# Kernel tuning notes

Hardware: AMD Instinct MI355X
Metric: run time of the kernel (lower is better)

The kernel has to match this reference:

```python
import jax, jax.numpy as jnp
import numpy as np

EPS = 1e-5  # BatchNorm eps (eval mode with running stats)

def conv1x1(x, w, b):
    # 1x1x1 Conv3d == channel matmul. x: (b,c,t,h,w), w: (o,c), b: (o,)
    return jnp.einsum('bcthw,oc->bothw', x, w) + b[None, :, None, None, None]

def pool122(x):
    # MaxPool3d kernel (1,2,2): max over non-overlapping 2x2 spatial windows
    b, c, t, h, w = x.shape
    return x.reshape(b, c, t, h // 2, 2, w // 2, 2).max(axis=(4, 6))

def setup_inputs() -> dict:
    key = jax.random.key(0)
    ks = jax.random.split(key, 13)
    C, Ci = 256, 128
    f32 = jnp.float32
    rn = lambda k, s, sc=1.0: jax.random.normal(k, s, dtype=f32) * sc
    return {
        'x': rn(ks[0], (4, C, 8, 32, 32)),
        'g_w': rn(ks[1], (Ci, C), 0.05), 'g_b': rn(ks[2], (Ci,), 0.05),
        'theta_w': rn(ks[3], (Ci, C), 0.05), 'theta_b': rn(ks[4], (Ci,), 0.05),
        'phi_w': rn(ks[5], (Ci, C), 0.05), 'phi_b': rn(ks[6], (Ci,), 0.05),
        'w_w': rn(ks[7], (C, Ci), 0.05), 'w_b': rn(ks[8], (C,), 0.05),
        'bn_gamma': rn(ks[9], (C,), 0.1) + 1.0,
        'bn_beta': rn(ks[10], (C,), 0.1),
        'bn_mean': rn(ks[11], (C,), 0.1),
        'bn_var': jax.random.uniform(ks[12], (C,), dtype=f32, minval=0.5, maxval=1.5),
    }

def reference(x, g_w, g_b, theta_w, theta_b, phi_w, phi_b, w_w, w_b,
              bn_gamma, bn_beta, bn_mean, bn_var):
    b = x.shape[0]
    ci = g_w.shape[0]
    # g, phi: conv then (1,2,2) maxpool (sub_sample=True)
    g_x = pool122(conv1x1(x, g_w, g_b)).reshape(b, ci, -1).transpose(0, 2, 1)      # (b, Nkv, ci)
    theta_x = conv1x1(x, theta_w, theta_b).reshape(b, ci, -1).transpose(0, 2, 1)   # (b, Nq, ci)
    phi_x = pool122(conv1x1(x, phi_w, phi_b)).reshape(b, ci, -1)                    # (b, ci, Nkv)
    f = jnp.einsum('bnc,bcm->bnm', theta_x, phi_x)                                  # (b, Nq, Nkv)
    attn = jax.nn.softmax(f, axis=-1)
    yy = jnp.einsum('bnm,bmc->bnc', attn, g_x)                                      # (b, Nq, ci)
    yy = yy.transpose(0, 2, 1).reshape(b, ci, *x.shape[2:])                         # (b, ci, t, h, w)
    wy = conv1x1(yy, w_w, w_b)
    # BatchNorm3d in eval mode with running stats
    scale = bn_gamma * jax.lax.rsqrt(bn_var + EPS)
    wy = wy * scale[None, :, None, None, None] + (bn_beta - bn_mean * scale)[None, :, None, None, None]
    return wy + x
```

## Files before the change

kernel.cpp:

```cpp
#include <hip/hip_runtime.h>
#include <hip/hip_bf16.h>

typedef __bf16 bf16x8 __attribute__((ext_vector_type(8)));
typedef __bf16 bf16x4 __attribute__((ext_vector_type(4)));
typedef __bf16 bf16x2 __attribute__((ext_vector_type(2)));
typedef float  f32x4  __attribute__((ext_vector_type(4)));

#define NB   4
#define C_   256
#define CI_  128
#define NSP  8192
#define NKV  2048
#define KVT  32
#define NT   (NKV/KVT)

__device__ __forceinline__ void gload_lds16(const void* g, void* l) {
    __builtin_amdgcn_global_load_lds(
        (const __attribute__((address_space(1))) void*)(unsigned long long)(uintptr_t)g,
        (__attribute__((address_space(3))) void*)(unsigned)(uintptr_t)l,
        16, 0, 0);
}

__global__ __launch_bounds__(256) void prep_kernel(
    const float* __restrict__ g_w,  const float* __restrict__ g_b,
    const float* __restrict__ th_w, const float* __restrict__ th_b,
    const float* __restrict__ ph_w, const float* __restrict__ ph_b,
    const float* __restrict__ w_w,  const float* __restrict__ w_b,
    const float* __restrict__ bn_g, const float* __restrict__ bn_be,
    const float* __restrict__ bn_m, const float* __restrict__ bn_v,
    __bf16* __restrict__ w_all, __bf16* __restrict__ w2,
    float* __restrict__ b_all, float* __restrict__ bnA, float* __restrict__ bnB)
{
    int idx = blockIdx.x * 256 + threadIdx.x;
    if (idx < 98304) {
        int o = idx >> 8, c = idx & 255;
        float v;
        if (o < 128)      v = th_w[o*256 + c];
        else if (o < 256) v = ph_w[(o-128)*256 + c];
        else              v = g_w[(o-256)*256 + c];
        w_all[idx] = (__bf16)v;
    } else if (idx < 131072) {
        int j = idx - 98304;
        w2[j] = (__bf16)w_w[j];
    } else if (idx < 131456) {
        int k = idx - 131072;
        float v;
        if (k < 128) v = th_b[k]; else if (k < 256) v = ph_b[k-128]; else v = g_b[k-256];
        b_all[k] = v;
    } else if (idx < 131712) {
        int m = idx - 131456;
        float sc = bn_g[m] * rsqrtf(bn_v[m] + 1e-5f);
        bnA[m] = sc;
        bnB[m] = w_b[m]*sc + bn_be[m] - bn_m[m]*sc;
    }
}

__global__ __launch_bounds__(256, 2) void proj_kernel(
    const float* __restrict__ x, const __bf16* __restrict__ w_all,
    const float* __restrict__ b_all,
    __bf16* __restrict__ Q, __bf16* __restrict__ K, __bf16* __restrict__ VT)
{
    const int b    = blockIdx.x >> 7;
    const int tile = blockIdx.x & 127;
    const int n0   = tile * 64;
    const int w    = threadIdx.x >> 6;
    const int lane = threadIdx.x & 63;
    const int lq   = lane & 15;
    const int g    = lane >> 4;

    const float* xb = x + b * (C_ * NSP);

    f32x4 acc[4][6];
    #pragma unroll
    for (int a = 0; a < 4; ++a)
        #pragma unroll
        for (int o = 0; o < 6; ++o) acc[a][o] = (f32x4){0.f,0.f,0.f,0.f};

    #pragma unroll 1
    for (int ck = 0; ck < 8; ++ck) {
        const int cbase = ck*32 + g*8;
        bf16x8 afr[4];
        #pragma unroll
        for (int nf = 0; nf < 4; ++nf) {
            const int n = n0 + nf*16 + lq;
            const float* xp = xb + cbase*NSP + n;
            bf16x8 v;
            #pragma unroll
            for (int e = 0; e < 8; ++e) v[e] = (__bf16)xp[e*NSP];
            afr[nf] = v;
        }
        #pragma unroll
        for (int oi = 0; oi < 6; ++oi) {
            const int orow = (w*6 + oi)*16 + lq;
            bf16x8 bfr = *(const bf16x8*)(w_all + orow*256 + cbase);
            #pragma unroll
            for (int nf = 0; nf < 4; ++nf)
                acc[nf][oi] = __builtin_amdgcn_mfma_f32_16x16x32_bf16(afr[nf], bfr, acc[nf][oi], 0,0,0);
        }
    }

    const int t  = n0 >> 10;
    const int h0 = (n0 & 1023) >> 5;
    const int kvrow0 = t*256 + (h0 >> 1)*16;

    #pragma unroll
    for (int oi = 0; oi < 6; ++oi) {
        const int ocol = (w*6 + oi)*16 + lq;
        const float bias = b_all[ocol];
        float v[4][4];
        #pragma unroll
        for (int nf = 0; nf < 4; ++nf)
            #pragma unroll
            for (int i = 0; i < 4; ++i) v[nf][i] = acc[nf][oi][i] + bias;

        const int seg = ocol >> 7;
        const int ol  = ocol & 127;
        if (seg == 0) {
            #pragma unroll
            for (int nf = 0; nf < 4; ++nf)
                #pragma unroll
                for (int i = 0; i < 4; ++i) {
                    int n = n0 + nf*16 + g*4 + i;
                    Q[(b*NSP + n)*CI_ + ol] = (__bf16)v[nf][i];
                }
        } else if (seg == 1) {
            #pragma unroll
            for (int nfp = 0; nfp < 2; ++nfp)
                #pragma unroll
                for (int j = 0; j < 2; ++j) {
                    float pv = fmaxf(fmaxf(v[nfp][2*j], v[nfp][2*j+1]),
                                     fmaxf(v[nfp+2][2*j], v[nfp+2][2*j+1]));
                    int wp = nfp*8 + g*2 + j;
                    K[(b*NKV + kvrow0 + wp)*CI_ + ol] = (__bf16)pv;
                }
        } else {
            #pragma unroll
            for (int nfp = 0; nfp < 2; ++nfp) {
                bf16x2 pk;
                #pragma unroll
                for (int j = 0; j < 2; ++j) {
                    float pv = fmaxf(fmaxf(v[nfp][2*j], v[nfp][2*j+1]),
                                     fmaxf(v[nfp+2][2*j], v[nfp+2][2*j+1]));
                    pk[j] = (__bf16)pv;
                }
                int wp = nfp*8 + g*2;
                *(bf16x2*)(VT + (b*CI_ + ol)*NKV + kvrow0 + wp) = pk;
            }
        }
    }
}

__global__ __launch_bounds__(256, 2) void attn_kernel(
    const __bf16* __restrict__ Q, const __bf16* __restrict__ K,
    const __bf16* __restrict__ VT, __bf16* __restrict__ yy)
{
    __shared__ __bf16 kbuf[3][32*128];
    __shared__ __bf16 vbuf[3][128*32];
    __shared__ __bf16 plds[4][16][40];

    const int b    = blockIdx.x >> 7;
    const int qt   = blockIdx.x & 127;
    const int w    = threadIdx.x >> 6;
    const int lane = threadIdx.x & 63;
    const int lq   = lane & 15;
    const int g    = lane >> 4;
    const int q0   = qt*64 + w*16;
    const float LOG2E = 1.4426950408889634f;

    bf16x8 qf[4];
    const __bf16* qrow = Q + (size_t)(b*NSP + q0 + lq)*CI_;
    #pragma unroll
    for (int kk = 0; kk < 4; ++kk) qf[kk] = *(const bf16x8*)(qrow + kk*32 + g*8);

    float m_run = -1e30f, l_run = 0.f;
    f32x4 oacc[8];
    #pragma unroll
    for (int d = 0; d < 8; ++d) oacc[d] = (f32x4){0.f,0.f,0.f,0.f};

    const __bf16* Kb0 = K  + (size_t)b*NKV*CI_;
    const __bf16* Vb0 = VT + (size_t)b*CI_*NKV;
    __bf16* pw = &plds[w][0][0];

    auto stage = [&](int bi, int kv0) {
        #pragma unroll
        for (int j = 0; j < 2; ++j) {
            int o   = w*2048 + j*1024 + lane*16;
            int row = o >> 8;
            int c   = (o & 255) ^ ((row & 7) << 4);
            const __bf16* src = Kb0 + (size_t)(kv0 + row)*CI_ + (c >> 1);
            gload_lds16(src, (char*)&kbuf[bi][0] + w*2048 + j*1024);
        }
        #pragma unroll
        for (int j = 0; j < 2; ++j) {
            int o    = w*2048 + j*1024 + lane*16;
            int row  = o >> 6;
            int slot = (o >> 4) & 3;
            int kc   = slot ^ ((row >> 1) & 3);
            const __bf16* src = Vb0 + (size_t)row*NKV + kv0 + kc*8;
            gload_lds16(src, (char*)&vbuf[bi][0] + w*2048 + j*1024);
        }
    };

    stage(0, 0);
    stage(1, KVT);

    for (int t = 0; t < NT; ++t) {
        asm volatile("s_waitcnt vmcnt(4)" ::: "memory");
        __builtin_amdgcn_s_barrier();
        __builtin_amdgcn_sched_barrier(0);

        {
            int tn = t + 2;
            int kvn = (tn < NT ? tn : NT-1) * KVT;
            stage(tn % 3, kvn);
        }

        const int bi = t % 3;
        const char* kb = (const char*)&kbuf[bi][0];
        const char* vb = (const char*)&vbuf[bi][0];

        f32x4 facc[2] = {(f32x4){0.f,0.f,0.f,0.f}, (f32x4){0.f,0.f,0.f,0.f}};
        __builtin_amdgcn_s_setprio(1);
        #pragma unroll
        for (int kk = 0; kk < 4; ++kk) {
            #pragma unroll
            for (int nf = 0; nf < 2; ++nf) {
                int row = nf*16 + lq;
                int c   = (kk*64 + g*16) ^ ((row & 7) << 4);
                bf16x8 kf = *(const bf16x8*)(kb + row*256 + c);
                facc[nf] = __builtin_amdgcn_mfma_f32_16x16x32_bf16(kf, qf[kk], facc[nf], 0,0,0);
            }
        }
        __builtin_amdgcn_s_setprio(0);

        float m0 = fmaxf(fmaxf(facc[0][0], facc[0][1]), fmaxf(facc[0][2], facc[0][3]));
        float m1 = fmaxf(fmaxf(facc[1][0], facc[1][1]), fmaxf(facc[1][2], facc[1][3]));
        float pmax = fmaxf(m0, m1);
        pmax = fmaxf(pmax, __shfl_xor(pmax, 16, 64));
        pmax = fmaxf(pmax, __shfl_xor(pmax, 32, 64));
        if (!__all(pmax - m_run <= 8.f)) {
            float mnew = fmaxf(m_run, pmax);
            float corr = __builtin_amdgcn_exp2f((m_run - mnew) * LOG2E);
            l_run *= corr;
            #pragma unroll
            for (int d = 0; d < 8; ++d) {
                oacc[d][0] *= corr; oacc[d][1] *= corr;
                oacc[d][2] *= corr; oacc[d][3] *= corr;
            }
            m_run = mnew;
        }
        float p[8];
        #pragma unroll
        for (int nf = 0; nf < 2; ++nf)
            #pragma unroll
            for (int i = 0; i < 4; ++i)
                p[nf*4+i] = __builtin_amdgcn_exp2f((facc[nf][i] - m_run) * LOG2E);
        float ps = ((p[0]+p[1]) + (p[2]+p[3])) + ((p[4]+p[5]) + (p[6]+p[7]));
        ps += __shfl_xor(ps, 16, 64);
        ps += __shfl_xor(ps, 32, 64);
        l_run += ps;

        #pragma unroll
        for (int nf = 0; nf < 2; ++nf) {
            bf16x4 pk;
            #pragma unroll
            for (int i = 0; i < 4; ++i) pk[i] = (__bf16)p[nf*4+i];
            *(bf16x4*)(pw + lq*40 + nf*16 + g*4) = pk;
        }
        bf16x8 pb = *(const bf16x8*)(pw + lq*40 + g*8);

        __builtin_amdgcn_s_setprio(1);
        #pragma unroll
        for (int df = 0; df < 8; ++df) {
            int row = df*16 + lq;
            int cb  = (g*16) ^ (((row >> 1) & 3) << 4);
            bf16x8 vf = *(const bf16x8*)(vb + row*64 + cb);
            oacc[df] = __builtin_amdgcn_mfma_f32_16x16x32_bf16(vf, pb, oacc[df], 0,0,0);
        }
        __builtin_amdgcn_s_setprio(0);
    }

    float inv = 1.f / l_run;
    __bf16* yrow = yy + (size_t)(b*NSP + q0 + lq)*CI_;
    #pragma unroll
    for (int df = 0; df < 8; ++df) {
        bf16x4 ov;
        #pragma unroll
        for (int i = 0; i < 4; ++i) ov[i] = (__bf16)(oacc[df][i] * inv);
        *(bf16x4*)(yrow + df*16 + g*4) = ov;
    }
}

__global__ __launch_bounds__(256, 2) void out_kernel(
    const __bf16* __restrict__ yy, const __bf16* __restrict__ w2,
    const float* __restrict__ bnA, const float* __restrict__ bnB,
    const float* __restrict__ x, float* __restrict__ out)
{
    const int b    = blockIdx.x >> 7;
    const int tile = blockIdx.x & 127;
    const int n0   = tile * 64;
    const int w    = threadIdx.x >> 6;
    const int lane = threadIdx.x & 63;
    const int lq   = lane & 15;
    const int g    = lane >> 4;

    f32x4 acc[4][4];
    #pragma unroll
    for (int a = 0; a < 4; ++a)
        #pragma unroll
        for (int o = 0; o < 4; ++o) acc[a][o] = (f32x4){0.f,0.f,0.f,0.f};

    #pragma unroll
    for (int kk = 0; kk < 4; ++kk) {
        bf16x8 bfr[4];
        #pragma unroll
        for (int nf = 0; nf < 4; ++nf)
            bfr[nf] = *(const bf16x8*)(yy + (size_t)(b*NSP + n0 + nf*16 + lq)*CI_ + kk*32 + g*8);
        #pragma unroll
        for (int cf = 0; cf < 4; ++cf) {
            const int corow = (w*4 + cf)*16 + lq;
            bf16x8 afr = *(const bf16x8*)(w2 + corow*CI_ + kk*32 + g*8);
            #pragma unroll
            for (int nf = 0; nf < 4; ++nf)
                acc[cf][nf] = __builtin_amdgcn_mfma_f32_16x16x32_bf16(afr, bfr[nf], acc[cf][nf], 0,0,0);
        }
    }

    #pragma unroll
    for (int cf = 0; cf < 4; ++cf) {
        #pragma unroll
        for (int i = 0; i < 4; ++i) {
            int co = (w*4 + cf)*16 + g*4 + i;
            float A = bnA[co], Bv = bnB[co];
            #pragma unroll
            for (int nf = 0; nf < 4; ++nf) {
                int n = n0 + nf*16 + lq;
                size_t idx = (size_t)(b*C_ + co)*NSP + n;
                out[idx] = acc[cf][nf][i]*A + Bv + x[idx];
            }
        }
    }
}

extern "C" void kernel_launch(void* const* d_in, const int* in_sizes, int n_in,
                              void* d_out, int out_size, void* d_ws, size_t ws_size,
                              hipStream_t stream)
{
    const float* x    = (const float*)d_in[0];
    const float* g_w  = (const float*)d_in[1];
    const float* g_b  = (const float*)d_in[2];
    const float* th_w = (const float*)d_in[3];
    const float* th_b = (const float*)d_in[4];
    const float* ph_w = (const float*)d_in[5];
    const float* ph_b = (const float*)d_in[6];
    const float* w_w  = (const float*)d_in[7];
    const float* w_b  = (const float*)d_in[8];
    const float* bn_g = (const float*)d_in[9];
    const float* bn_be= (const float*)d_in[10];
    const float* bn_m = (const float*)d_in[11];
    const float* bn_v = (const float*)d_in[12];

    char* ws = (char*)d_ws;
    size_t off = 0;
    auto alloc = [&](size_t bytes) -> void* {
        void* p = ws + off;
        off += (bytes + 255) & ~(size_t)255;
        return p;
    };
    __bf16* w_all = (__bf16*)alloc(384*256*2);
    __bf16* w2    = (__bf16*)alloc(256*128*2);
    float*  b_all = (float*) alloc(384*4);
    float*  bnA   = (float*) alloc(256*4);
    float*  bnB   = (float*) alloc(256*4);
    __bf16* Qb    = (__bf16*)alloc((size_t)NB*NSP*CI_*2);
    __bf16* Kb    = (__bf16*)alloc((size_t)NB*NKV*CI_*2);
    __bf16* Vt    = (__bf16*)alloc((size_t)NB*CI_*NKV*2);
    __bf16* yyb   = (__bf16*)alloc((size_t)NB*NSP*CI_*2);

    prep_kernel<<<515, 256, 0, stream>>>(g_w, g_b, th_w, th_b, ph_w, ph_b, w_w, w_b,
                                         bn_g, bn_be, bn_m, bn_v,
                                         w_all, w2, b_all, bnA, bnB);
    proj_kernel<<<512, 256, 0, stream>>>(x, w_all, b_all, Qb, Kb, Vt);
    attn_kernel<<<512, 256, 0, stream>>>(Qb, Kb, Vt, yyb);
    out_kernel <<<512, 256, 0, stream>>>(yyb, w2, bnA, bnB, x, (float*)d_out);
}
```

Before: 198.6 us.

## Double query rows per wave in attention and vectorize output epilogue

Each attention wave now handles 32 query rows in two 16-row sub-tiles, so every K and V fragment read from LDS feeds two MFMAs. This halves the grid to 256 blocks and drops to one block per CU, doubling K/V reuse per LDS stage. In the output kernel the MFMA operands are swapped so each lane holds four consecutive spatial positions, which allows 16-byte vectorized loads of x and stores of out. The cost is higher register pressure and fewer blocks than CUs on MI355X, which reduces occupancy and latency hiding.

```diff
diff --git a/kernel.cpp b/kernel.cpp
--- a/kernel.cpp
+++ b/kernel.cpp
@@ -150,32 +150,37 @@
     }
 }
 
-__global__ __launch_bounds__(256, 2) void attn_kernel(
+__global__ __launch_bounds__(256, 1) void attn_kernel(
     const __bf16* __restrict__ Q, const __bf16* __restrict__ K,
     const __bf16* __restrict__ VT, __bf16* __restrict__ yy)
 {
     __shared__ __bf16 kbuf[3][32*128];
     __shared__ __bf16 vbuf[3][128*32];
-    __shared__ __bf16 plds[4][16][40];
-
-    const int b    = blockIdx.x >> 7;
-    const int qt   = blockIdx.x & 127;
+    __shared__ __bf16 plds[4][32][40];
+
+    const int b    = blockIdx.x >> 6;
+    const int qt   = blockIdx.x & 63;
     const int w    = threadIdx.x >> 6;
     const int lane = threadIdx.x & 63;
     const int lq   = lane & 15;
     const int g    = lane >> 4;
-    const int q0   = qt*64 + w*16;
+    const int q0   = qt*128 + w*32;
     const float LOG2E = 1.4426950408889634f;
 
-    bf16x8 qf[4];
-    const __bf16* qrow = Q + (size_t)(b*NSP + q0 + lq)*CI_;
-    #pragma unroll
-    for (int kk = 0; kk < 4; ++kk) qf[kk] = *(const bf16x8*)(qrow + kk*32 + g*8);
-
-    float m_run = -1e30f, l_run = 0.f;
-    f32x4 oacc[8];
-    #pragma unroll
-    for (int d = 0; d < 8; ++d) oacc[d] = (f32x4){0.f,0.f,0.f,0.f};
+    bf16x8 qf[2][4];
+    #pragma unroll
+    for (int s = 0; s < 2; ++s) {
+        const __bf16* qrow = Q + (size_t)(b*NSP + q0 + s*16 + lq)*CI_;
+        #pragma unroll
+        for (int kk = 0; kk < 4; ++kk) qf[s][kk] = *(const bf16x8*)(qrow + kk*32 + g*8);
+    }
+
+    float m_run[2] = {-1e30f, -1e30f}, l_run[2] = {0.f, 0.f};
+    f32x4 oacc[2][8];
+    #pragma unroll
+    for (int s = 0; s < 2; ++s)
+        #pragma unroll
+        for (int d = 0; d < 8; ++d) oacc[s][d] = (f32x4){0.f,0.f,0.f,0.f};
 
     const __bf16* Kb0 = K  + (size_t)b*NKV*CI_;
     const __bf16* Vb0 = VT + (size_t)b*CI_*NKV;
@@ -219,7 +224,11 @@
         const char* kb = (const char*)&kbuf[bi][0];
         const char* vb = (const char*)&vbuf[bi][0];
 
-        f32x4 facc[2] = {(f32x4){0.f,0.f,0.f,0.f}, (f32x4){0.f,0.f,0.f,0.f}};
+        f32x4 facc[2][2];
+        #pragma unroll
+        for (int s = 0; s < 2; ++s)
+            #pragma unroll
+            for (int nf = 0; nf < 2; ++nf) facc[s][nf] = (f32x4){0.f,0.f,0.f,0.f};
         __builtin_amdgcn_s_setprio(1);
         #pragma unroll
         for (int kk = 0; kk < 4; ++kk) {
@@ -228,46 +237,52 @@
                 int row = nf*16 + lq;
                 int c   = (kk*64 + g*16) ^ ((row & 7) << 4);
                 bf16x8 kf = *(const bf16x8*)(kb + row*256 + c);
-                facc[nf] = __builtin_amdgcn_mfma_f32_16x16x32_bf16(kf, qf[kk], facc[nf], 0,0,0);
+                facc[0][nf] = __builtin_amdgcn_mfma_f32_16x16x32_bf16(kf, qf[0][kk], facc[0][nf], 0,0,0);
+                facc[1][nf] = __builtin_amdgcn_mfma_f32_16x16x32_bf16(kf, qf[1][kk], facc[1][nf], 0,0,0);
             }
         }
         __builtin_amdgcn_s_setprio(0);
 
-        float m0 = fmaxf(fmaxf(facc[0][0], facc[0][1]), fmaxf(facc[0][2], facc[0][3]));
-        float m1 = fmaxf(fmaxf(facc[1][0], facc[1][1]), fmaxf(facc[1][2], facc[1][3]));
-        float pmax = fmaxf(m0, m1);
-        pmax = fmaxf(pmax, __shfl_xor(pmax, 16, 64));
-        pmax = fmaxf(pmax, __shfl_xor(pmax, 32, 64));
-        if (!__all(pmax - m_run <= 8.f)) {
-            float mnew = fmaxf(m_run, pmax);
-            float corr = __builtin_amdgcn_exp2f((m_run - mnew) * LOG2E);
-            l_run *= corr;
-            #pragma unroll
-            for (int d = 0; d < 8; ++d) {
-                oacc[d][0] *= corr; oacc[d][1] *= corr;
-                oacc[d][2] *= corr; oacc[d][3] *= corr;
+        #pragma unroll
+        for (int s = 0; s < 2; ++s) {
+            float m0 = fmaxf(fmaxf(facc[s][0][0], facc[s][0][1]), fmaxf(facc[s][0][2], facc[s][0][3]));
+            float m1 = fmaxf(fmaxf(facc[s][1][0], facc[s][1][1]), fmaxf(facc[s][1][2], facc[s][1][3]));
+            float pmax = fmaxf(m0, m1);
+            pmax = fmaxf(pmax, __shfl_xor(pmax, 16, 64));
+            pmax = fmaxf(pmax, __shfl_xor(pmax, 32, 64));
+            if (!__all(pmax - m_run[s] <= 8.f)) {
+                float mnew = fmaxf(m_run[s], pmax);
+                float corr = __builtin_amdgcn_exp2f((m_run[s] - mnew) * LOG2E);
+                l_run[s] *= corr;
+                #pragma unroll
+                for (int d = 0; d < 8; ++d) {
+                    oacc[s][d][0] *= corr; oacc[s][d][1] *= corr;
+                    oacc[s][d][2] *= corr; oacc[s][d][3] *= corr;
+                }
+                m_run[s] = mnew;
             }
-            m_run = mnew;
-        }
-        float p[8];
-        #pragma unroll
-        for (int nf = 0; nf < 2; ++nf)
-            #pragma unroll
-            for (int i = 0; i < 4; ++i)
-                p[nf*4+i] = __builtin_amdgcn_exp2f((facc[nf][i] - m_run) * LOG2E);
-        float ps = ((p[0]+p[1]) + (p[2]+p[3])) + ((p[4]+p[5]) + (p[6]+p[7]));
-        ps += __shfl_xor(ps, 16, 64);
-        ps += __shfl_xor(ps, 32, 64);
-        l_run += ps;
-
-        #pragma unroll
-        for (int nf = 0; nf < 2; ++nf) {
-            bf16x4 pk;
-            #pragma unroll
-            for (int i = 0; i < 4; ++i) pk[i] = (__bf16)p[nf*4+i];
-            *(bf16x4*)(pw + lq*40 + nf*16 + g*4) = pk;
-        }
-        bf16x8 pb = *(const bf16x8*)(pw + lq*40 + g*8);
+            float p[8];
+            #pragma unroll
+            for (int nf = 0; nf < 2; ++nf)
+                #pragma unroll
+                for (int i = 0; i < 4; ++i)
+                    p[nf*4+i] = __builtin_amdgcn_exp2f((facc[s][nf][i] - m_run[s]) * LOG2E);
+            float ps = ((p[0]+p[1]) + (p[2]+p[3])) + ((p[4]+p[5]) + (p[6]+p[7]));
+            ps += __shfl_xor(ps, 16, 64);
+            ps += __shfl_xor(ps, 32, 64);
+            l_run[s] += ps;
+            #pragma unroll
+            for (int nf = 0; nf < 2; ++nf) {
+                bf16x4 pk;
+                #pragma unroll
+                for (int i = 0; i < 4; ++i) pk[i] = (__bf16)p[nf*4+i];
+                *(bf16x4*)(pw + (s*16 + lq)*40 + nf*16 + g*4) = pk;
+            }
+        }
+        bf16x8 pb[2];
+        #pragma unroll
+        for (int s = 0; s < 2; ++s)
+            pb[s] = *(const bf16x8*)(pw + (s*16 + lq)*40 + g*8);
 
         __builtin_amdgcn_s_setprio(1);
         #pragma unroll
@@ -275,19 +290,23 @@
             int row = df*16 + lq;
             int cb  = (g*16) ^ (((row >> 1) & 3) << 4);
             bf16x8 vf = *(const bf16x8*)(vb + row*64 + cb);
-            oacc[df] = __builtin_amdgcn_mfma_f32_16x16x32_bf16(vf, pb, oacc[df], 0,0,0);
+            oacc[0][df] = __builtin_amdgcn_mfma_f32_16x16x32_bf16(vf, pb[0], oacc[0][df], 0,0,0);
+            oacc[1][df] = __builtin_amdgcn_mfma_f32_16x16x32_bf16(vf, pb[1], oacc[1][df], 0,0,0);
         }
         __builtin_amdgcn_s_setprio(0);
     }
 
-    float inv = 1.f / l_run;
-    __bf16* yrow = yy + (size_t)(b*NSP + q0 + lq)*CI_;
-    #pragma unroll
-    for (int df = 0; df < 8; ++df) {
-        bf16x4 ov;
-        #pragma unroll
-        for (int i = 0; i < 4; ++i) ov[i] = (__bf16)(oacc[df][i] * inv);
-        *(bf16x4*)(yrow + df*16 + g*4) = ov;
+    #pragma unroll
+    for (int s = 0; s < 2; ++s) {
+        float inv = 1.f / l_run[s];
+        __bf16* yrow = yy + (size_t)(b*NSP + q0 + s*16 + lq)*CI_;
+        #pragma unroll
+        for (int df = 0; df < 8; ++df) {
+            bf16x4 ov;
+            #pragma unroll
+            for (int i = 0; i < 4; ++i) ov[i] = (__bf16)(oacc[s][df][i] * inv);
+            *(bf16x4*)(yrow + df*16 + g*4) = ov;
+        }
     }
 }
 
@@ -312,32 +331,33 @@
 
     #pragma unroll
     for (int kk = 0; kk < 4; ++kk) {
-        bf16x8 bfr[4];
+        bf16x8 afr[4];
         #pragma unroll
         for (int nf = 0; nf < 4; ++nf)
-            bfr[nf] = *(const bf16x8*)(yy + (size_t)(b*NSP + n0 + nf*16 + lq)*CI_ + kk*32 + g*8);
+            afr[nf] = *(const bf16x8*)(yy + (size_t)(b*NSP + n0 + nf*16 + lq)*CI_ + kk*32 + g*8);
         #pragma unroll
         for (int cf = 0; cf < 4; ++cf) {
             const int corow = (w*4 + cf)*16 + lq;
-            bf16x8 afr = *(const bf16x8*)(w2 + corow*CI_ + kk*32 + g*8);
+            bf16x8 bfr = *(const bf16x8*)(w2 + corow*CI_ + kk*32 + g*8);
             #pragma unroll
             for (int nf = 0; nf < 4; ++nf)
-                acc[cf][nf] = __builtin_amdgcn_mfma_f32_16x16x32_bf16(afr, bfr[nf], acc[cf][nf], 0,0,0);
+                acc[cf][nf] = __builtin_amdgcn_mfma_f32_16x16x32_bf16(afr[nf], bfr, acc[cf][nf], 0,0,0);
         }
     }
 
     #pragma unroll
     for (int cf = 0; cf < 4; ++cf) {
-        #pragma unroll
-        for (int i = 0; i < 4; ++i) {
-            int co = (w*4 + cf)*16 + g*4 + i;
-            float A = bnA[co], Bv = bnB[co];
-            #pragma unroll
-            for (int nf = 0; nf < 4; ++nf) {
-                int n = n0 + nf*16 + lq;
-                size_t idx = (size_t)(b*C_ + co)*NSP + n;
-                out[idx] = acc[cf][nf][i]*A + Bv + x[idx];
-            }
+        const int co = (w*4 + cf)*16 + lq;
+        const float A = bnA[co], Bv = bnB[co];
+        #pragma unroll
+        for (int nf = 0; nf < 4; ++nf) {
+            const int n = n0 + nf*16 + g*4;
+            size_t idx = (size_t)(b*C_ + co)*NSP + n;
+            f32x4 xv = *(const f32x4*)(x + idx);
+            f32x4 ov;
+            #pragma unroll
+            for (int i = 0; i < 4; ++i) ov[i] = acc[cf][nf][i]*A + Bv + xv[i];
+            *(f32x4*)(out + idx) = ov;
         }
     }
 }
@@ -381,6 +401,6 @@
                                          bn_g, bn_be, bn_m, bn_v,
                                          w_all, w2, b_all, bnA, bnB);
     proj_kernel<<<512, 256, 0, stream>>>(x, w_all, b_all, Qb, Kb, Vt);
-    attn_kernel<<<512, 256, 0, stream>>>(Qb, Kb, Vt, yyb);
+    attn_kernel<<<256, 256, 0, stream>>>(Qb, Kb, Vt, yyb);
     out_kernel <<<512, 256, 0, stream>>>(yyb, w2, bnA, bnB, x, (float*)d_out);
 }
```

New measurement: 218.8 us. 10.2% more time.
